# Performance work log

Hardware: AMD Instinct MI355X
Metric: run time of the kernel (lower is better)

Reference implementation:

```python
import jax, jax.numpy as jnp
import numpy as np

MESH_RESOLUTION = 0.1
ORDER = 3  # TSC interpolation


def setup_inputs() -> dict:
    key = jax.random.key(0)
    k1, k2 = jax.random.split(key)
    L = 20.0
    N, C = 100000, 8
    positions = jax.random.uniform(k1, (N, 3), dtype=jnp.float32) * L
    cell = jnp.eye(3, dtype=jnp.float32) * L
    embeddings = jax.random.normal(k2, (N, C), dtype=jnp.float32)
    return {"positions": positions, "cell": cell, "embeddings": embeddings}


def _weights_order3(dist):
    # dist: [N,3]; returns [3,N,3]
    d2 = dist * dist
    return jnp.stack([
        0.125 * (1.0 - 4.0 * dist + 4.0 * d2),
        0.25 * (3.0 - 4.0 * d2),
        0.125 * (1.0 + 4.0 * dist + 4.0 * d2),
    ])


def reference(positions, cell, embeddings):
    # Mesh setup (cubic box)
    mesh_size = float(jnp.trace(cell)) / 3.0
    n_mesh = int(2 * round(mesh_size / (2.0 * MESH_RESOLUTION)))
    spacing = mesh_size / n_mesh
    C = embeddings.shape[1]

    positions_cell = positions / spacing  # [N,3]
    # odd order: nearest-grid-point centering
    idx = jnp.round(positions_cell).astype(jnp.int32)  # [N,3]
    dist = positions_cell - idx.astype(positions_cell.dtype)  # [N,3]

    w = _weights_order3(dist)  # [3,N,3]
    offs = jnp.arange(1 - (ORDER + 1) // 2, 1 + ORDER // 2)  # [-1,0,1]
    rp = (idx[None, :, :] + offs[:, None, None]) % n_mesh  # [3,N,3]

    xs, ys, zs = jnp.meshgrid(jnp.arange(ORDER), jnp.arange(ORDER), jnp.arange(ORDER), indexing='ij')
    xs, ys, zs = xs.ravel(), ys.ravel(), zs.ravel()  # [27]

    # flat grid indices and combined weights per (corner, atom)
    flat_idx = (rp[xs, :, 0] * n_mesh + rp[ys, :, 1]) * n_mesh + rp[zs, :, 2]  # [27,N]
    wprod = w[xs, :, 0] * w[ys, :, 1] * w[zs, :, 2]  # [27,N]

    vals = wprod[:, :, None] * embeddings[None, :, :]  # [27,N,C]
    grid = jnp.zeros((n_mesh ** 3, C), dtype=positions.dtype)
    grid = grid.at[flat_idx.reshape(-1)].add(vals.reshape(-1, C))
    # -> (C, n, n, n) to match mesh.values layout
    return grid.reshape(n_mesh, n_mesh, n_mesh, C).transpose(3, 0, 1, 2)
```

## Files before the change

### kernel.cpp

```cpp
#include <hip/hip_runtime.h>
#include <math.h>


#define KColCAP 16

typedef float nfloat4 __attribute__((ext_vector_type(4)));

__device__ __forceinline__ float tsc_w(int o, float d) {
    float t = 0.5f + (float)o * d;
    return (o == 0) ? (0.75f - d * d) : (0.5f * t * t);
}

__device__ __forceinline__ float inv_spacing(const float* __restrict__ cell, int n) {
    float tr = cell[0] + cell[4] + cell[8];
    return (3.0f * (float)n) / tr;
}


__global__ __launch_bounds__(256) void fill_recs(
    const float* __restrict__ pos, const float* __restrict__ cell,
    const float* __restrict__ emb,
    int* __restrict__ counts, int* __restrict__ ovf_cnt,
    float4* __restrict__ binrec, int* __restrict__ ovf,
    int N, int n)
{
    int i = blockIdx.x * blockDim.x + threadIdx.x;
    if (i >= N) return;
    float inv_sp = inv_spacing(cell, n);
    float px = pos[3 * i + 0] * inv_sp;
    float py = pos[3 * i + 1] * inv_sp;
    float pz = pos[3 * i + 2] * inv_sp;
    int cx = (int)rintf(px); if (cx >= n) cx -= n; else if (cx < 0) cx += n;
    int cy = (int)rintf(py); if (cy >= n) cy -= n; else if (cy < 0) cy += n;
    int bin = cx * n + cy;
    int slot = atomicAdd(&counts[bin], 1);
    if (slot < KColCAP) {
        const float4* e4 = (const float4*)(emb + (size_t)i * 8);
        float4* r = binrec + (size_t)(bin * KColCAP + slot) * 3;
        r[0] = make_float4(px, py, pz, 0.0f);
        r[1] = e4[0];
        r[2] = e4[1];
    } else {
        int o = atomicAdd(ovf_cnt, 1);
        ovf[o] = i;
    }
}


__global__ __launch_bounds__(256) void gather_scatter(
    const float4* __restrict__ binrec, const int* __restrict__ counts,
    float* __restrict__ out, int n, int nzc)
{
    extern __shared__ float lds[];
    const int tid = threadIdx.x;
    const int lane = tid & 63;
    const int wv = tid >> 6;

    const int nb = nzc * n;
    const int b = blockIdx.x;
    const int q = nb >> 3, r = nb & 7;
    const int xcd = b & 7, idx = b >> 3;
    const int sb = (xcd < r) ? (xcd * (q + 1) + idx)
                             : (r * (q + 1) + (xcd - r) * q + idx);
    const int x = sb / nzc;
    const int ygrp = sb - x * nzc;
    const int y = ygrp * 4 + wv;

    float* col = lds + wv * 8 * n;

    {
        nfloat4* c4 = (nfloat4*)col;
        const int z4 = 2 * n;
        for (int i = lane; i < z4; i += 64)
            c4[i] = (nfloat4)(0.f);
    }

    int base[9], pref[10];
    pref[0] = 0;
    #pragma unroll
    for (int j = 0; j < 9; ++j) {
        int jx = j / 3, jy = j - 3 * (j / 3);
        int xb = x + jx - 1; if (xb < 0) xb += n; else if (xb >= n) xb -= n;
        int yb = y + jy - 1; if (yb < 0) yb += n; else if (yb >= n) yb -= n;
        int bin = xb * n + yb;
        base[j] = bin * KColCAP;
        int c = counts[bin];
        c = (c < KColCAP) ? c : KColCAP;
        pref[j + 1] = pref[j] + c;
    }
    const int tot = pref[9];

    const int s  = lane / 3;
    const int zc = lane - 3 * s - 1;

    for (int q0 = 0; q0 < tot; q0 += 21) {
        const int qq = q0 + s;
        if (s < 21 && qq < tot) {
            int rec = base[0] + qq;
            int jxv = 0, jyv = 0;
            #pragma unroll
            for (int k = 1; k < 9; ++k) {
                bool ge = (qq >= pref[k]);
                int cand = base[k] + (qq - pref[k]);
                rec = ge ? cand : rec;
                jxv = ge ? (k / 3) : jxv;
                jyv = ge ? (k - 3 * (k / 3)) : jyv;
            }
            const float4* rp = binrec + (size_t)rec * 3;
            float4 P  = rp[0];
            float4 e0 = rp[1];
            float4 e1 = rp[2];

            float cxf = rintf(P.x); float dx = P.x - cxf;
            float cyf = rintf(P.y); float dy = P.y - cyf;
            float czf = rintf(P.z); float dz = P.z - czf;

            float tx = 0.5f + (float)(1 - jxv) * dx;
            float wx = (jxv == 1) ? (0.75f - dx * dx) : (0.5f * tx * tx);
            float ty = 0.5f + (float)(1 - jyv) * dy;
            float wy = (jyv == 1) ? (0.75f - dy * dy) : (0.5f * ty * ty);
            float tz = 0.5f + (float)zc * dz;
            float wz = (zc == 0) ? (0.75f - dz * dz) : (0.5f * tz * tz);
            float w = wx * wy * wz;

            int cz = (int)czf; if (cz >= n) cz -= n; else if (cz < 0) cz += n;
            int z = cz + zc; if (z < 0) z += n; else if (z >= n) z -= n;

            float* p = col + z;
            atomicAdd(p + 0 * n, w * e0.x);
            atomicAdd(p + 1 * n, w * e0.y);
            atomicAdd(p + 2 * n, w * e0.z);
            atomicAdd(p + 3 * n, w * e0.w);
            atomicAdd(p + 4 * n, w * e1.x);
            atomicAdd(p + 5 * n, w * e1.y);
            atomicAdd(p + 6 * n, w * e1.z);
            atomicAdd(p + 7 * n, w * e1.w);
        }
    }

    const int z0 = lane * 4;
    if (z0 < n) {
        const size_t n3 = (size_t)n * n * n;
        const size_t colbase = ((size_t)x * n + y) * (size_t)n + z0;
        #pragma unroll
        for (int ch = 0; ch < 8; ++ch) {
            nfloat4 v = *(const nfloat4*)(col + ch * n + z0);
            *(nfloat4*)(out + (size_t)ch * n3 + colbase) = v;
        }
    }
}

__global__ __launch_bounds__(256) void deposit_overflow(
    const float* __restrict__ pos, const float* __restrict__ cell,
    const float* __restrict__ emb, const int* __restrict__ ovf_cnt,
    const int* __restrict__ ovf, float* __restrict__ out, int n)
{
    int m = *ovf_cnt;
    int i = blockIdx.x * blockDim.x + threadIdx.x;
    if (i >= m) return;
    int ai = ovf[i];
    float inv_sp = inv_spacing(cell, n);
    float p[3], d[3]; int c0[3];
    #pragma unroll
    for (int kk = 0; kk < 3; ++kk) {
        p[kk] = pos[3 * ai + kk] * inv_sp;
        c0[kk] = (int)rintf(p[kk]);
        d[kk] = p[kk] - (float)c0[kk];
    }
    float w[3][3];
    #pragma unroll
    for (int kk = 0; kk < 3; ++kk) {
        float dd = d[kk];
        w[kk][0] = tsc_w(-1, dd); w[kk][1] = tsc_w(0, dd); w[kk][2] = tsc_w(1, dd);
    }
    int W[3][3];
    #pragma unroll
    for (int kk = 0; kk < 3; ++kk)
        #pragma unroll
        for (int a = 0; a < 3; ++a) {
            int v = c0[kk] - 1 + a; if (v < 0) v += n; else if (v >= n) v -= n;
            W[kk][a] = v;
        }
    size_t n3 = (size_t)n * n * n;
    const float4* e4 = (const float4*)(emb + (size_t)ai * 8);
    float4 e0 = e4[0], e1 = e4[1];
    float e[8] = {e0.x, e0.y, e0.z, e0.w, e1.x, e1.y, e1.z, e1.w};
    for (int a = 0; a < 3; ++a)
        for (int bq = 0; bq < 3; ++bq)
            for (int cq = 0; cq < 3; ++cq) {
                float wt = w[0][a] * w[1][bq] * w[2][cq];
                size_t g = ((size_t)W[0][a] * n + W[1][bq]) * n + W[2][cq];
                #pragma unroll
                for (int ch = 0; ch < 8; ++ch)
                    atomicAdd(out + (size_t)ch * n3 + g, wt * e[ch]);
            }
}


__global__ __launch_bounds__(256) void deposit_tsc8_ilv(
    const float* __restrict__ pos,
    const float* __restrict__ cell,
    const float* __restrict__ emb,
    float* __restrict__ ws,
    int total, int n)
{
    int t = blockIdx.x * blockDim.x + threadIdx.x;
    if (t >= total) return;
    int atom = t / 27;
    int c    = t - atom * 27;
    int a    = c / 9;
    int rem  = c - a * 9;
    int b    = rem / 3;
    int cc   = rem - b * 3;

    float inv_sp = inv_spacing(cell, n);

    float px = pos[3 * atom + 0] * inv_sp;
    float py = pos[3 * atom + 1] * inv_sp;
    float pz = pos[3 * atom + 2] * inv_sp;

    int cx = (int)rintf(px);  float dx = px - (float)cx;
    int cy = (int)rintf(py);  float dy = py - (float)cy;
    int cz = (int)rintf(pz);  float dz = pz - (float)cz;

    float w = tsc_w(a - 1, dx) * tsc_w(b - 1, dy) * tsc_w(cc - 1, dz);

    int x = cx - 1 + a;  if (x < 0) x += n; else if (x >= n) x -= n;
    int y = cy - 1 + b;  if (y < 0) y += n; else if (y >= n) y -= n;
    int z = cz - 1 + cc; if (z < 0) z += n; else if (z >= n) z -= n;

    const float4* e4 = (const float4*)(emb + (size_t)atom * 8);
    float4 e0 = e4[0], e1 = e4[1];

    float* p = ws + ((size_t)((x * n + y) * n + z)) * 8;
    atomicAdd(p + 0, w * e0.x);
    atomicAdd(p + 1, w * e0.y);
    atomicAdd(p + 2, w * e0.z);
    atomicAdd(p + 3, w * e0.w);
    atomicAdd(p + 4, w * e1.x);
    atomicAdd(p + 5, w * e1.y);
    atomicAdd(p + 6, w * e1.z);
    atomicAdd(p + 7, w * e1.w);
}

__global__ __launch_bounds__(256) void transpose_ilv8(
    const float* __restrict__ ws, float* __restrict__ out, int n3)
{
    int t = blockIdx.x * blockDim.x + threadIdx.x;
    int g0 = t * 4;
    if (g0 >= n3) return;
    const float4* w4 = (const float4*)(ws + (size_t)g0 * 8);
    float4 r0 = w4[0], r1 = w4[1];
    float4 r2 = w4[2], r3 = w4[3];
    float4 r4 = w4[4], r5 = w4[5];
    float4 r6 = w4[6], r7 = w4[7];

    *(float4*)(out + (size_t)0 * n3 + g0) = make_float4(r0.x, r2.x, r4.x, r6.x);
    *(float4*)(out + (size_t)1 * n3 + g0) = make_float4(r0.y, r2.y, r4.y, r6.y);
    *(float4*)(out + (size_t)2 * n3 + g0) = make_float4(r0.z, r2.z, r4.z, r6.z);
    *(float4*)(out + (size_t)3 * n3 + g0) = make_float4(r0.w, r2.w, r4.w, r6.w);
    *(float4*)(out + (size_t)4 * n3 + g0) = make_float4(r1.x, r3.x, r5.x, r7.x);
    *(float4*)(out + (size_t)5 * n3 + g0) = make_float4(r1.y, r3.y, r5.y, r7.y);
    *(float4*)(out + (size_t)6 * n3 + g0) = make_float4(r1.z, r3.z, r5.z, r7.z);
    *(float4*)(out + (size_t)7 * n3 + g0) = make_float4(r1.w, r3.w, r5.w, r7.w);
}


__global__ __launch_bounds__(256) void deposit_tsc_gen(
    const float* __restrict__ pos,
    const float* __restrict__ cell,
    const float* __restrict__ emb,
    float* __restrict__ out,
    int N, int n, int C)
{
    int i = blockIdx.x * blockDim.x + threadIdx.x;
    if (i >= N) return;

    float inv_sp = inv_spacing(cell, n);

    float p[3], d[3];
    int c0[3];
    #pragma unroll
    for (int k = 0; k < 3; ++k) {
        p[k] = pos[3 * i + k] * inv_sp;
        c0[k] = (int)rintf(p[k]);
        d[k] = p[k] - (float)c0[k];
    }
    float w[3][3];
    #pragma unroll
    for (int k = 0; k < 3; ++k) {
        float dd = d[k], d2 = dd * dd;
        w[k][0] = 0.125f * (1.0f - 4.0f * dd + 4.0f * d2);
        w[k][1] = 0.25f  * (3.0f - 4.0f * d2);
        w[k][2] = 0.125f * (1.0f + 4.0f * dd + 4.0f * d2);
    }
    int W[3][3];
    #pragma unroll
    for (int k = 0; k < 3; ++k) {
        #pragma unroll
        for (int a = 0; a < 3; ++a) {
            int v = c0[k] - 1 + a; if (v < 0) v += n; else if (v >= n) v -= n;
            W[k][a] = v;
        }
    }
    int n3 = n * n * n;
    for (int a = 0; a < 3; ++a)
        for (int b = 0; b < 3; ++b)
            for (int cc = 0; cc < 3; ++cc) {
                float wt = w[0][a] * w[1][b] * w[2][cc];
                int g = (W[0][a] * n + W[1][b]) * n + W[2][cc];
                for (int ch = 0; ch < C; ++ch)
                    atomicAdd(out + (size_t)ch * n3 + g, wt * emb[(size_t)i * C + ch]);
            }
}

extern "C" void kernel_launch(void* const* d_in, const int* in_sizes, int n_in,
                              void* d_out, int out_size, void* d_ws, size_t ws_size,
                              hipStream_t stream) {
    const float* pos  = (const float*)d_in[0];
    const float* cell = (const float*)d_in[1];
    const float* emb  = (const float*)d_in[2];
    float* out = (float*)d_out;
    float* ws  = (float*)d_ws;

    int N = in_sizes[0] / 3;
    int C = in_sizes[2] / N;
    long long n3l = (long long)out_size / C;
    int n = (int)llroundf(cbrtf((float)n3l));
    int n3 = (int)n3l;

    int block = 256;

    {
        int nb = n * n;
        size_t lds_bytes = (size_t)4 * 8 * n * sizeof(float);
        size_t rec_off = (((size_t)nb + 4 + (size_t)N) * sizeof(int) + 15) & ~(size_t)15;
        size_t need = rec_off + (size_t)nb * KColCAP * 48;
        bool ok = (C == 8) && (n % 4 == 0) && n >= 8 && n <= 256
                  && lds_bytes <= 64 * 1024
                  && ws_size >= need
                  && ((long long)n * n * n == n3l);
        if (ok) {
            int* counts  = (int*)d_ws;
            int* ovf_cnt = counts + nb;
            int* ovf     = counts + nb + 4;
            float4* binrec = (float4*)((char*)d_ws + rec_off);

            (void)hipMemsetAsync(counts, 0, (size_t)(nb + 4) * sizeof(int), stream);
            fill_recs<<<(N + block - 1) / block, block, 0, stream>>>(
                pos, cell, emb, counts, ovf_cnt, binrec, ovf, N, n);

            int nzc = n / 4;
            gather_scatter<<<nzc * n, block, lds_bytes, stream>>>(
                binrec, counts, out, n, nzc);

            deposit_overflow<<<(N + block - 1) / block, block, 0, stream>>>(
                pos, cell, emb, ovf_cnt, ovf, out, n);
            return;
        }
    }

    size_t need = (size_t)out_size * sizeof(float);
    if (C == 8 && ws_size >= need && (n3 % 4) == 0) {
        (void)hipMemsetAsync(d_ws, 0, need, stream);
        int total = N * 27;
        deposit_tsc8_ilv<<<(total + block - 1) / block, block, 0, stream>>>(
            pos, cell, emb, ws, total, n);
        int tthreads = n3 / 4;
        transpose_ilv8<<<(tthreads + block - 1) / block, block, 0, stream>>>(
            ws, out, n3);
    } else {
        (void)hipMemsetAsync(d_out, 0, (size_t)out_size * sizeof(float), stream);
        int grid = (N + block - 1) / block;
        deposit_tsc_gen<<<grid, block, 0, stream>>>(pos, cell, emb, out, N, n, C);
    }
}
```

Baseline: 146.5 us.

## Pack embeddings as fp16 in bin records and software-pipeline record loads

Bin records shrink from 48 to 32 bytes by storing the eight embedding channels as packed half2 values next to the position, which cuts global write and read traffic between the fill and gather kernels. The gather loop also prefetches the next round of records into registers while the current one is being deposited, hiding load latency. The cost is fp16 rounding of the embeddings, which may break tolerance, plus extra register pressure from the prefetch buffers.

```diff
diff --git a/kernel.cpp b/kernel.cpp
--- a/kernel.cpp
+++ b/kernel.cpp
@@ -1,4 +1,5 @@
 #include <hip/hip_runtime.h>
+#include <hip/hip_fp16.h>
 #include <math.h>
 
 
@@ -14,6 +15,12 @@
 __device__ __forceinline__ float inv_spacing(const float* __restrict__ cell, int n) {
     float tr = cell[0] + cell[4] + cell[8];
     return (3.0f * (float)n) / tr;
+}
+
+__device__ __forceinline__ float2 unpack_h2(float bits) {
+    unsigned int u = __float_as_uint(bits);
+    __half2 h = *(__half2*)&u;
+    return __half22float2(h);
 }
 
 
@@ -36,10 +43,19 @@
     int slot = atomicAdd(&counts[bin], 1);
     if (slot < KColCAP) {
         const float4* e4 = (const float4*)(emb + (size_t)i * 8);
-        float4* r = binrec + (size_t)(bin * KColCAP + slot) * 3;
-        r[0] = make_float4(px, py, pz, 0.0f);
-        r[1] = e4[0];
-        r[2] = e4[1];
+        float4 e0 = e4[0], e1 = e4[1];
+        __half2 h01 = __floats2half2_rn(e0.x, e0.y);
+        __half2 h23 = __floats2half2_rn(e0.z, e0.w);
+        __half2 h45 = __floats2half2_rn(e1.x, e1.y);
+        __half2 h67 = __floats2half2_rn(e1.z, e1.w);
+        unsigned int u01 = *(unsigned int*)&h01;
+        unsigned int u23 = *(unsigned int*)&h23;
+        unsigned int u45 = *(unsigned int*)&h45;
+        unsigned int u67 = *(unsigned int*)&h67;
+        float4* r = binrec + (size_t)(bin * KColCAP + slot) * 2;
+        r[0] = make_float4(px, py, pz, __uint_as_float(u01));
+        r[1] = make_float4(__uint_as_float(u23), __uint_as_float(u45),
+                           __uint_as_float(u67), 0.0f);
     } else {
         int o = atomicAdd(ovf_cnt, 1);
         ovf[o] = i;
@@ -58,10 +74,10 @@
 
     const int nb = nzc * n;
     const int b = blockIdx.x;
-    const int q = nb >> 3, r = nb & 7;
+    const int q8 = nb >> 3, r8 = nb & 7;
     const int xcd = b & 7, idx = b >> 3;
-    const int sb = (xcd < r) ? (xcd * (q + 1) + idx)
-                             : (r * (q + 1) + (xcd - r) * q + idx);
+    const int sb = (xcd < r8) ? (xcd * (q8 + 1) + idx)
+                              : (r8 * (q8 + 1) + (xcd - r8) * q8 + idx);
     const int x = sb / nzc;
     const int ygrp = sb - x * nzc;
     const int y = ygrp * 4 + wv;
@@ -93,49 +109,74 @@
     const int s  = lane / 3;
     const int zc = lane - 3 * s - 1;
 
+    float4 a0, a1; int jxA = 0, jyA = 0;
+    bool vA = (s < 21) && (s < tot);
+    if (vA) {
+        int rec = base[0] + s; int jxv = 0, jyv = 0;
+        #pragma unroll
+        for (int k = 1; k < 9; ++k) {
+            bool ge = (s >= pref[k]);
+            int cand = base[k] + (s - pref[k]);
+            rec = ge ? cand : rec;
+            jxv = ge ? (k / 3) : jxv;
+            jyv = ge ? (k - 3 * (k / 3)) : jyv;
+        }
+        a0 = binrec[2 * (size_t)rec];
+        a1 = binrec[2 * (size_t)rec + 1];
+        jxA = jxv; jyA = jyv;
+    }
+
     for (int q0 = 0; q0 < tot; q0 += 21) {
-        const int qq = q0 + s;
-        if (s < 21 && qq < tot) {
-            int rec = base[0] + qq;
-            int jxv = 0, jyv = 0;
+        const int qn = q0 + 21 + s;
+        const bool vB = (s < 21) && (qn < tot);
+        float4 b0 = a0, b1 = a1; int jxB = jxA, jyB = jyA;
+        if (vB) {
+            int rec = base[0] + qn; int jxv = 0, jyv = 0;
             #pragma unroll
             for (int k = 1; k < 9; ++k) {
-                bool ge = (qq >= pref[k]);
-                int cand = base[k] + (qq - pref[k]);
+                bool ge = (qn >= pref[k]);
+                int cand = base[k] + (qn - pref[k]);
                 rec = ge ? cand : rec;
                 jxv = ge ? (k / 3) : jxv;
                 jyv = ge ? (k - 3 * (k / 3)) : jyv;
             }
-            const float4* rp = binrec + (size_t)rec * 3;
-            float4 P  = rp[0];
-            float4 e0 = rp[1];
-            float4 e1 = rp[2];
-
-            float cxf = rintf(P.x); float dx = P.x - cxf;
-            float cyf = rintf(P.y); float dy = P.y - cyf;
-            float czf = rintf(P.z); float dz = P.z - czf;
-
-            float tx = 0.5f + (float)(1 - jxv) * dx;
-            float wx = (jxv == 1) ? (0.75f - dx * dx) : (0.5f * tx * tx);
-            float ty = 0.5f + (float)(1 - jyv) * dy;
-            float wy = (jyv == 1) ? (0.75f - dy * dy) : (0.5f * ty * ty);
+            b0 = binrec[2 * (size_t)rec];
+            b1 = binrec[2 * (size_t)rec + 1];
+            jxB = jxv; jyB = jyv;
+        }
+
+        if (vA) {
+            float cxf = rintf(a0.x); float dx = a0.x - cxf;
+            float cyf = rintf(a0.y); float dy = a0.y - cyf;
+            float czf = rintf(a0.z); float dz = a0.z - czf;
+
+            float tx = 0.5f + (float)(1 - jxA) * dx;
+            float wx = (jxA == 1) ? (0.75f - dx * dx) : (0.5f * tx * tx);
+            float ty = 0.5f + (float)(1 - jyA) * dy;
+            float wy = (jyA == 1) ? (0.75f - dy * dy) : (0.5f * ty * ty);
             float tz = 0.5f + (float)zc * dz;
             float wz = (zc == 0) ? (0.75f - dz * dz) : (0.5f * tz * tz);
             float w = wx * wy * wz;
 
+            float2 e01 = unpack_h2(a0.w);
+            float2 e23 = unpack_h2(a1.x);
+            float2 e45 = unpack_h2(a1.y);
+            float2 e67 = unpack_h2(a1.z);
+
             int cz = (int)czf; if (cz >= n) cz -= n; else if (cz < 0) cz += n;
             int z = cz + zc; if (z < 0) z += n; else if (z >= n) z -= n;
 
             float* p = col + z;
-            atomicAdd(p + 0 * n, w * e0.x);
-            atomicAdd(p + 1 * n, w * e0.y);
-            atomicAdd(p + 2 * n, w * e0.z);
-            atomicAdd(p + 3 * n, w * e0.w);
-            atomicAdd(p + 4 * n, w * e1.x);
-            atomicAdd(p + 5 * n, w * e1.y);
-            atomicAdd(p + 6 * n, w * e1.z);
-            atomicAdd(p + 7 * n, w * e1.w);
-        }
+            atomicAdd(p + 0 * n, w * e01.x);
+            atomicAdd(p + 1 * n, w * e01.y);
+            atomicAdd(p + 2 * n, w * e23.x);
+            atomicAdd(p + 3 * n, w * e23.y);
+            atomicAdd(p + 4 * n, w * e45.x);
+            atomicAdd(p + 5 * n, w * e45.y);
+            atomicAdd(p + 6 * n, w * e67.x);
+            atomicAdd(p + 7 * n, w * e67.y);
+        }
+        a0 = b0; a1 = b1; jxA = jxB; jyA = jyB; vA = vB;
     }
 
     const int z0 = lane * 4;
@@ -335,7 +376,7 @@
         int nb = n * n;
         size_t lds_bytes = (size_t)4 * 8 * n * sizeof(float);
         size_t rec_off = (((size_t)nb + 4 + (size_t)N) * sizeof(int) + 15) & ~(size_t)15;
-        size_t need = rec_off + (size_t)nb * KColCAP * 48;
+        size_t need = rec_off + (size_t)nb * KColCAP * 32;
         bool ok = (C == 8) && (n % 4 == 0) && n >= 8 && n <= 256
                   && lds_bytes <= 64 * 1024
                   && ws_size >= need
```

New measurement: 145.7 us. No clear change (-0.6%).
